# Kernel tuning notes

Hardware: AMD Instinct MI355X
Metric: run time of the kernel (lower is better)

Reference implementation:

```python
import jax, jax.numpy as jnp
import numpy as np

L_LAYERS = 6   # decoder layers
N_HEAD = 8
NUM_PAIR = 100  # num_pair_queries
LN_EPS = 1e-5


def _ln(x, g, b):
    m = x.mean(-1, keepdims=True)
    v = ((x - m) ** 2).mean(-1, keepdims=True)
    return (x - m) / jnp.sqrt(v + LN_EPS) * g + b


def _mlp2(x, w1, b1, w2, b2):
    return jax.nn.relu(x @ w1.T + b1) @ w2.T + b2


def _mha(q, k, v, in_w, in_b, out_w, out_b):
    # torch nn.MultiheadAttention (batch_first, eval mode) equivalent
    C = q.shape[-1]
    dh = C // N_HEAD
    wq, wk, wv = jnp.split(in_w, 3, axis=0)
    bq, bk, bv = jnp.split(in_b, 3, axis=0)
    def heads(x, w, b):
        y = x @ w.T + b
        return y.reshape(x.shape[0], x.shape[1], N_HEAD, dh).transpose(0, 2, 1, 3)
    qh, kh, vh = heads(q, wq, bq), heads(k, wk, bk), heads(v, wv, bv)
    att = jax.nn.softmax(jnp.einsum('bhqd,bhkd->bhqk', qh, kh) * (1.0 / np.sqrt(dh)), axis=-1)
    out = jnp.einsum('bhqk,bhkd->bhqd', att, vh).transpose(0, 2, 1, 3).reshape(q.shape[0], q.shape[1], C)
    return out @ out_w.T + out_b


def reference(hs_last, mem, mem_pos, sub_boxes, obj_boxes,
              su_w1, su_b1, su_w2, su_b2, ou_w1, ou_b1, ou_w2, ou_b2,
              pm_w1, pm_b1, pm_w2, pm_b2, sp_w1, sp_b1, sp_w2, sp_b2,
              sa_in_w, sa_in_b, sa_out_w, sa_out_b, ca_in_w, ca_in_b, ca_out_w, ca_out_b,
              l1_w, l1_b, l2_w, l2_b, n1_g, n1_b, n2_g, n2_b, n3_g, n3_b):
    B, Q, C = hs_last.shape
    N = Q // 2
    hsp = hs_last.reshape(B, N, 2, C)
    sub_feat, obj_feat = hsp[:, :, 0, :], hsp[:, :, 1, :]

    # --- HumanObjectPairLearner.select_topk_indices (mapper='identity') ---
    sub_emb = _mlp2(sub_feat, su_w1, su_b1, su_w2, su_b2)
    obj_emb = _mlp2(obj_feat, ou_w1, ou_b1, ou_w2, ou_b2)
    sub_emb = sub_emb / (jnp.linalg.norm(sub_emb, axis=-1, keepdims=True) + 1e-6)
    obj_emb = obj_emb / (jnp.linalg.norm(obj_emb, axis=-1, keepdims=True) + 1e-6)
    importance = jnp.einsum('bnc,bmc->bnm', sub_emb, obj_emb)  # [B, N, N]
    K = min(NUM_PAIR, N * N)
    _, idx = jax.lax.top_k(importance.reshape(B, N * N), K)
    sub_pos, obj_pos = idx // N, idx % N  # [B, K]

    # --- build_pair_queries: gather selected sub/obj features ---
    sel_sub = jnp.take_along_axis(sub_feat, sub_pos[:, :, None], axis=1)  # [B, K, C]
    sel_obj = jnp.take_along_axis(obj_feat, obj_pos[:, :, None], axis=1)
    pair_q = _mlp2(jnp.concatenate([sel_sub, sel_obj], axis=-1), pm_w1, pm_b1, pm_w2, pm_b2)

    # --- PairSpatialEncoding ---
    sp = _mlp2(jnp.concatenate([sub_boxes, obj_boxes], axis=-1), sp_w1, sp_b1, sp_w2, sp_b2)

    # --- LocalityAwareInteractionDecoder (eval mode: dropout = identity) ---
    q = pair_q
    k_mem = mem + mem_pos
    for i in range(L_LAYERS):
        q_sp = q + sp
        sa = _mha(q_sp, q_sp, q_sp, sa_in_w[i], sa_in_b[i], sa_out_w[i], sa_out_b[i])
        q = _ln(q + sa, n1_g[i], n1_b[i])
        # original: cross_attn(cat([q, sp], dim=1), ...)[:, :K] -- attention is
        # per-query, so slicing after equals running cross-attn with q alone.
        ca = _mha(q, k_mem, mem, ca_in_w[i], ca_in_b[i], ca_out_w[i], ca_out_b[i])
        q = _ln(q + ca, n2_g[i], n2_b[i])
        ffn = jax.nn.relu(q @ l1_w[i].T + l1_b[i]) @ l2_w[i].T + l2_b[i]
        q = _ln(q + ffn, n3_g[i], n3_b[i])
    return q


def setup_inputs() -> dict:
    B, N, C, M, F, L = 32, 100, 256, 4096, 2048, L_LAYERS
    K = NUM_PAIR
    keys = iter(jax.random.split(jax.random.key(0), 80))
    def nrm(shape, s=1.0):
        return jax.random.normal(next(keys), shape, jnp.float32) * s
    w = lambda shape: nrm(shape, 0.02)
    return {
        'hs_last': nrm((B, 2 * N, C)),
        'mem': nrm((B, M, C)),
        'mem_pos': nrm((B, M, C)),
        'sub_boxes': jax.random.uniform(next(keys), (B, K, 4), jnp.float32),
        'obj_boxes': jax.random.uniform(next(keys), (B, K, 4), jnp.float32),
        'su_w1': w((C, C)), 'su_b1': jnp.zeros((C,)), 'su_w2': w((C, C)), 'su_b2': jnp.zeros((C,)),
        'ou_w1': w((C, C)), 'ou_b1': jnp.zeros((C,)), 'ou_w2': w((C, C)), 'ou_b2': jnp.zeros((C,)),
        'pm_w1': w((C, 2 * C)), 'pm_b1': jnp.zeros((C,)), 'pm_w2': w((C, C)), 'pm_b2': jnp.zeros((C,)),
        'sp_w1': w((C, 8)), 'sp_b1': jnp.zeros((C,)), 'sp_w2': w((C, C)), 'sp_b2': jnp.zeros((C,)),
        'sa_in_w': w((L, 3 * C, C)), 'sa_in_b': jnp.zeros((L, 3 * C)),
        'sa_out_w': w((L, C, C)), 'sa_out_b': jnp.zeros((L, C)),
        'ca_in_w': w((L, 3 * C, C)), 'ca_in_b': jnp.zeros((L, 3 * C)),
        'ca_out_w': w((L, C, C)), 'ca_out_b': jnp.zeros((L, C)),
        'l1_w': w((L, F, C)), 'l1_b': jnp.zeros((L, F)),
        'l2_w': w((L, C, F)), 'l2_b': jnp.zeros((L, C)),
        'n1_g': jnp.ones((L, C)), 'n1_b': jnp.zeros((L, C)),
        'n2_g': jnp.ones((L, C)), 'n2_b': jnp.zeros((L, C)),
        'n3_g': jnp.ones((L, C)), 'n3_b': jnp.zeros((L, C)),
    }
```

## Files before the change

kernel.cpp:

```cpp
#include <hip/hip_runtime.h>
#include <hip/hip_bf16.h>

#define Bb 32
#define Nn 100
#define Cc 256
#define Mm 4096
#define Ff 2048
#define Ll 6
#define Hh 8
#define DH 32
#define KP 100
#define TT (Bb*KP)
#define LNEPS 1e-5f
#define NCH 4
#define SUBK 128

typedef __hip_bfloat16 bf16;
typedef unsigned short ushort_t;
typedef __attribute__((ext_vector_type(8))) short short8v;
typedef __attribute__((ext_vector_type(4))) float f32x4;

union FragU { uint2 u2[2]; uint4 u4; short8v s8; };

__device__ __forceinline__ float bfu2f(unsigned short u) {
  union { unsigned u32; float f; } cv; cv.u32 = ((unsigned)u) << 16; return cv.f;
}
__device__ __forceinline__ unsigned short f2bf(float f) {
  union { float f; unsigned u; } c; c.f = f;
  unsigned r = c.u + 0x7FFF + ((c.u >> 16) & 1);
  return (unsigned short)(r >> 16);
}
__device__ __forceinline__ unsigned pack2(float a, float b) {
  return (unsigned)f2bf(a) | ((unsigned)f2bf(b) << 16);
}

__global__ __launch_bounds__(256) void gemm_kv(
    const bf16* __restrict__ Ak, const bf16* __restrict__ Wk,
    const float* __restrict__ bk, bf16* __restrict__ outK,
    const bf16* __restrict__ Avv, const bf16* __restrict__ Wv,
    const float* __restrict__ bv, bf16* __restrict__ outV,
    const float* __restrict__ Aq, const bf16* __restrict__ Wq,
    const float* __restrict__ bq, bf16* __restrict__ outQ)
{
  __shared__ ushort_t Ct[128*136];
  const int nwgK = ((Bb*Mm) >> 7) * 2;
  const int nwgQ = (TT >> 7) * 2;
  const int nwg = 2*nwgK + nwgQ;
  const int g = blockIdx.x;
  const int xcd = g & 7, lid = g >> 3;
  const int q8 = nwg >> 3, r8 = nwg & 7;
  int wgid = (xcd < r8 ? xcd*(q8+1) : r8*(q8+1) + (xcd - r8)*q8) + lid;
  int seg;
  const bf16* A = nullptr; const bf16* W; const float* bias; bf16* out;
  if (wgid < nwgK)        { seg = 0; A = Ak;  W = Wk; bias = bk; out = outK; }
  else if (wgid < 2*nwgK) { seg = 1; wgid -= nwgK;   A = Avv; W = Wv; bias = bv; out = outV; }
  else                    { seg = 2; wgid -= 2*nwgK; W = Wq; bias = bq; out = outQ; }
  const int ntile = wgid & 1, mtile = wgid >> 1;
  const int bm = mtile << 7, bn = ntile << 7;
  const int tid = threadIdx.x;
  const int w = tid >> 6, lane = tid & 63;
  const int lr = lane & 15, lg = lane >> 4;
  const int wm = w >> 1, wn = w & 1;

  f32x4 acc[4][4] = {};

  if (seg != 2) {
    #pragma unroll 2
    for (int k0 = 0; k0 < Cc; k0 += 32) {
      FragU a[4], b[4];
      #pragma unroll
      for (int mi = 0; mi < 4; ++mi)
        a[mi].u4 = *(const uint4*)(A + (size_t)(bm + wm*64 + mi*16 + lr)*Cc + k0 + lg*8);
      #pragma unroll
      for (int ni = 0; ni < 4; ++ni)
        b[ni].u4 = *(const uint4*)(W + (size_t)(bn + wn*64 + ni*16 + lr)*Cc + k0 + lg*8);
      #pragma unroll
      for (int ni = 0; ni < 4; ++ni)
        #pragma unroll
        for (int mi = 0; mi < 4; ++mi)
          acc[mi][ni] = __builtin_amdgcn_mfma_f32_16x16x32_bf16(a[mi].s8, b[ni].s8,
                                                                acc[mi][ni], 0, 0, 0);
    }
  } else {
    #pragma unroll 2
    for (int k0 = 0; k0 < Cc; k0 += 32) {
      FragU a[4], b[4];
      #pragma unroll
      for (int mi = 0; mi < 4; ++mi) {
        const float* ap = Aq + (size_t)(bm + wm*64 + mi*16 + lr)*Cc + k0 + lg*8;
        float4 f0 = *(const float4*)ap;
        float4 f1 = *(const float4*)(ap + 4);
        a[mi].u4.x = pack2(f0.x, f0.y); a[mi].u4.y = pack2(f0.z, f0.w);
        a[mi].u4.z = pack2(f1.x, f1.y); a[mi].u4.w = pack2(f1.z, f1.w);
      }
      #pragma unroll
      for (int ni = 0; ni < 4; ++ni)
        b[ni].u4 = *(const uint4*)(W + (size_t)(bn + wn*64 + ni*16 + lr)*Cc + k0 + lg*8);
      #pragma unroll
      for (int ni = 0; ni < 4; ++ni)
        #pragma unroll
        for (int mi = 0; mi < 4; ++mi)
          acc[mi][ni] = __builtin_amdgcn_mfma_f32_16x16x32_bf16(a[mi].s8, b[ni].s8,
                                                                acc[mi][ni], 0, 0, 0);
    }
  }

  const float scale = (seg == 2) ? 0.17677669529663687f : 1.f;
  #pragma unroll
  for (int ni = 0; ni < 4; ++ni) {
    int col = wn*64 + ni*16 + lr;
    float bvv = bias[bn + col];
    #pragma unroll
    for (int mi = 0; mi < 4; ++mi)
      #pragma unroll
      for (int r = 0; r < 4; ++r) {
        int rowl = wm*64 + mi*16 + lg*4 + r;
        Ct[rowl*136 + col] = f2bf((acc[mi][ni][r] + bvv) * scale);
      }
  }
  __syncthreads();
  for (int u = tid; u < 2048; u += 256) {
    int rowl = u >> 4, sub = u & 15;
    uint4 v = *(const uint4*)&Ct[rowl*136 + sub*8];
    int m = bm + rowl;
    int gcol = bn + sub*8;
    int h = gcol >> 5, dd = gcol & 31;
    if (seg != 2) {
      int bb = m >> 12, mm = m & 4095;
      *(uint4*)(out + (((size_t)bb*Hh + h)*Mm + mm)*DH + dd) = v;
    } else {
      int bb = m / KP, qq = m % KP;
      *(uint4*)(out + (((size_t)bb*Hh + h)*KP + qq)*DH + dd) = v;
    }
  }
}

template<int AT, bool RELU, int OM>
__global__ __launch_bounds__(256) void gemm_mfma(
    const void* __restrict__ Av, const float* __restrict__ A2,
    const bf16* __restrict__ W, const float* __restrict__ bias,
    void* __restrict__ out, int M, int N, int K)
{
  __shared__ ushort_t SM[2*128*72];
  ushort_t* As = SM;
  ushort_t* Bs = SM + 128*72;
  const int mt = M >> 7, nt = N >> 7;
  const int nwg = mt * nt;
  const int g = blockIdx.x;
  const int xcd = g & 7, lid = g >> 3;
  const int q8 = nwg >> 3, r8 = nwg & 7;
  int wgid = (xcd < r8 ? xcd*(q8+1) : r8*(q8+1) + (xcd - r8)*q8) + lid;
  const int ntile = wgid % nt, mtile = wgid / nt;
  const int bm = mtile << 7, bn = ntile << 7;
  const int tid = threadIdx.x;
  const int w = tid >> 6, lane = tid & 63;
  const int lr = lane & 15, lg = lane >> 4;
  const int wm = w >> 1, wn = w & 1;
  const float* Af = (const float*)Av;
  const bf16*  Ab = (const bf16*)Av;

  f32x4 acc[4][4] = {};

  for (int k0 = 0; k0 < K; k0 += 64) {
    __syncthreads();
    #pragma unroll
    for (int i = 0; i < 4; ++i) {
      int linear = i*256 + tid;
      int row = linear >> 3, c8 = linear & 7;
      uint4 packed;
      if (AT == 0) {
        const float* ap = Af + (size_t)(bm+row)*K + k0 + c8*8;
        float4 f0 = *(const float4*)ap;
        float4 f1 = *(const float4*)(ap+4);
        if (A2) {
          const float* ap2 = A2 + (size_t)(bm+row)*K + k0 + c8*8;
          float4 g0 = *(const float4*)ap2;
          float4 g1 = *(const float4*)(ap2+4);
          f0.x += g0.x; f0.y += g0.y; f0.z += g0.z; f0.w += g0.w;
          f1.x += g1.x; f1.y += g1.y; f1.z += g1.z; f1.w += g1.w;
        }
        packed.x = pack2(f0.x, f0.y); packed.y = pack2(f0.z, f0.w);
        packed.z = pack2(f1.x, f1.y); packed.w = pack2(f1.z, f1.w);
      } else {
        packed = *(const uint4*)(Ab + (size_t)(bm+row)*K + k0 + c8*8);
      }
      *(uint4*)&As[row*72 + c8*8] = packed;
      uint4 wb = *(const uint4*)(W + (size_t)(bn+row)*K + k0 + c8*8);
      *(uint4*)&Bs[row*72 + c8*8] = wb;
    }
    __syncthreads();
    #pragma unroll
    for (int kk = 0; kk < 64; kk += 32) {
      FragU a[4];
      #pragma unroll
      for (int mi = 0; mi < 4; ++mi)
        a[mi].u4 = *(const uint4*)&As[(wm*64 + mi*16 + lr)*72 + kk + lg*8];
      #pragma unroll
      for (int ni = 0; ni < 4; ++ni) {
        FragU bfr;
        bfr.u4 = *(const uint4*)&Bs[(wn*64 + ni*16 + lr)*72 + kk + lg*8];
        #pragma unroll
        for (int mi = 0; mi < 4; ++mi)
          acc[mi][ni] = __builtin_amdgcn_mfma_f32_16x16x32_bf16(a[mi].s8, bfr.s8,
                                                                acc[mi][ni], 0, 0, 0);
      }
    }
  }

  #pragma unroll
  for (int ni = 0; ni < 4; ++ni) {
    int col = bn + wn*64 + ni*16 + lr;
    float bv = bias ? bias[col] : 0.f;
    #pragma unroll
    for (int mi = 0; mi < 4; ++mi) {
      #pragma unroll
      for (int r = 0; r < 4; ++r) {
        int m = bm + wm*64 + mi*16 + lg*4 + r;
        float v = acc[mi][ni][r] + bv;
        if (RELU) v = fmaxf(v, 0.f);
        if (OM == 0) {
          ((float*)out)[(size_t)m*N + col] = v;
        } else if (OM == 1) {
          ((bf16*)out)[(size_t)m*N + col] = __float2bfloat16(v);
        } else {
          int bb = m / KP, qq = m % KP;
          int h = col >> 5, dd = col & 31;
          ((bf16*)out)[(((size_t)bb*Hh + h)*KP + qq)*DH + dd] =
              __float2bfloat16(v * 0.17677669529663687f);
        }
      }
    }
  }
}

template<int AT>
__global__ __launch_bounds__(512) void gemm_ln(
    const void* __restrict__ Av, const bf16* __restrict__ W,
    const float* __restrict__ bias, const float* __restrict__ resid,
    const float* __restrict__ gamma, const float* __restrict__ beta,
    float* __restrict__ out, int M, int K,
    const bf16* __restrict__ part, const float2* __restrict__ ml)
{
  __shared__ ushort_t As[16][72];
  __shared__ ushort_t Bs[256][72];
  __shared__ float redS[16][8];
  __shared__ float redQ[16][8];
  const int bm = blockIdx.x * 16;
  const int tid = threadIdx.x;
  const int w = tid >> 6, lane = tid & 63;
  const int lr = lane & 15, lg = lane >> 4;
  const float* Af = (const float*)Av;
  const bf16*  Ab = (const bf16*)Av;
  f32x4 acc[2] = {};

  for (int k0 = 0; k0 < K; k0 += 64) {
    __syncthreads();
    if (tid < 128) {
      int row = tid >> 3, c8 = tid & 7;
      uint4 packed;
      if (AT == 0) {
        const float* ap = Af + (size_t)(bm+row)*K + k0 + c8*8;
        float4 f0 = *(const float4*)ap;
        float4 f1 = *(const float4*)(ap+4);
        packed.x = pack2(f0.x, f0.y); packed.y = pack2(f0.z, f0.w);
        packed.z = pack2(f1.x, f1.y); packed.w = pack2(f1.z, f1.w);
      } else if (AT == 1) {
        packed = *(const uint4*)(Ab + (size_t)(bm+row)*K + k0 + c8*8);
      } else {
        int t = bm + row;
        int b = t / KP, q = t % KP;
        int ch0 = k0 + c8*8;
        int h = ch0 >> 5, d0 = ch0 & 31;
        int bh = b*Hh + h;
        float2 m0 = ml[((size_t)bh*NCH + 0)*KP + q];
        float2 m1 = ml[((size_t)bh*NCH + 1)*KP + q];
        float2 m2 = ml[((size_t)bh*NCH + 2)*KP + q];
        float2 m3 = ml[((size_t)bh*NCH + 3)*KP + q];
        float mm = fmaxf(fmaxf(m0.x, m1.x), fmaxf(m2.x, m3.x));
        float w0 = __expf(m0.x - mm), w1 = __expf(m1.x - mm);
        float w2 = __expf(m2.x - mm), w3 = __expf(m3.x - mm);
        float invL = 1.f / (m0.y*w0 + m1.y*w1 + m2.y*w2 + m3.y*w3);
        float o[8] = {};
        float wc[NCH] = { w0, w1, w2, w3 };
        #pragma unroll
        for (int c = 0; c < NCH; ++c) {
          uint4 pv = *(const uint4*)(part + (((size_t)bh*NCH + c)*KP + q)*DH + d0);
          const ushort_t* pe = (const ushort_t*)&pv;
          #pragma unroll
          for (int e = 0; e < 8; ++e) o[e] += wc[c] * bfu2f(pe[e]);
        }
        packed.x = pack2(o[0]*invL, o[1]*invL);
        packed.y = pack2(o[2]*invL, o[3]*invL);
        packed.z = pack2(o[4]*invL, o[5]*invL);
        packed.w = pack2(o[6]*invL, o[7]*invL);
      }
      *(uint4*)&As[row][c8*8] = packed;
    }
    #pragma unroll
    for (int i = 0; i < 4; ++i) {
      int linear = i*512 + tid;
      int row = linear >> 3, c8 = linear & 7;
      *(uint4*)&Bs[row][c8*8] = *(const uint4*)(W + (size_t)row*K + k0 + c8*8);
    }
    __syncthreads();
    #pragma unroll
    for (int kk = 0; kk < 64; kk += 32) {
      FragU a;
      a.u4 = *(const uint4*)&As[lr][kk + lg*8];
      #pragma unroll
      for (int ni = 0; ni < 2; ++ni) {
        FragU bfr;
        bfr.u4 = *(const uint4*)&Bs[w*32 + ni*16 + lr][kk + lg*8];
        acc[ni] = __builtin_amdgcn_mfma_f32_16x16x32_bf16(a.s8, bfr.s8, acc[ni], 0, 0, 0);
      }
    }
  }

  float x[2][4];
  #pragma unroll
  for (int r = 0; r < 4; ++r) {
    int row = bm + lg*4 + r;
    float s = 0.f, sq = 0.f;
    #pragma unroll
    for (int ni = 0; ni < 2; ++ni) {
      int col = w*32 + ni*16 + lr;
      float v = acc[ni][r] + bias[col] + resid[(size_t)row*Cc + col];
      x[ni][r] = v;
      s += v; sq += v*v;
    }
    #pragma unroll
    for (int m2 = 1; m2 < 16; m2 <<= 1) { s += __shfl_xor(s, m2); sq += __shfl_xor(sq, m2); }
    if (lr == 0) { redS[lg*4 + r][w] = s; redQ[lg*4 + r][w] = sq; }
  }
  __syncthreads();
  #pragma unroll
  for (int r = 0; r < 4; ++r) {
    int lrow = lg*4 + r;
    float ss = 0.f, sq = 0.f;
    #pragma unroll
    for (int j = 0; j < 8; ++j) { ss += redS[lrow][j]; sq += redQ[lrow][j]; }
    float mean = ss * (1.f/Cc);
    float var = sq * (1.f/Cc) - mean*mean;
    float inv = rsqrtf(var + LNEPS);
    #pragma unroll
    for (int ni = 0; ni < 2; ++ni) {
      int col = w*32 + ni*16 + lr;
      out[(size_t)(bm+lrow)*Cc + col] = (x[ni][r] - mean)*inv*gamma[col] + beta[col];
    }
  }
}

#define NSEG 9
struct CvtDesc {
  const float* src[NSEG];
  bf16* dst[NSEG];
  int n4[NSEG];
  int total4;
};
__global__ __launch_bounds__(256) void cvt_multi(CvtDesc d) {
  int stride = gridDim.x * blockDim.x;
  for (int i = blockIdx.x*256 + threadIdx.x; i < d.total4; i += stride) {
    int seg = 0, off = i;
    while (off >= d.n4[seg]) { off -= d.n4[seg]; ++seg; }
    float4 f = *(const float4*)(d.src[seg] + (size_t)off*4);
    uint2 p; p.x = pack2(f.x, f.y); p.y = pack2(f.z, f.w);
    *(uint2*)(d.dst[seg] + (size_t)off*4) = p;
  }
}

__global__ __launch_bounds__(256) void prep_mem(const float4* __restrict__ mem4,
                                                const float4* __restrict__ pos4,
                                                uint2* __restrict__ kb2,
                                                uint2* __restrict__ vb2) {
  int i = blockIdx.x*256 + threadIdx.x;
  const int stride = 8192*256;
  #pragma unroll
  for (int t = 0; t < 4; ++t) {
    int j = i + t*stride;
    float4 a = mem4[j];
    float4 p = pos4[j];
    uint2 vv; vv.x = pack2(a.x, a.y); vv.y = pack2(a.z, a.w);
    uint2 kv; kv.x = pack2(a.x + p.x, a.y + p.y); kv.y = pack2(a.z + p.z, a.w + p.w);
    vb2[j] = vv;
    kb2[j] = kv;
  }
}

template<bool RELU>
__global__ __launch_bounds__(256) void gemm_nt(
    const float* __restrict__ A0, const float* __restrict__ W0,
    const float* __restrict__ b0, float* __restrict__ o0,
    const float* __restrict__ A1, const float* __restrict__ W1,
    const float* __restrict__ b1, float* __restrict__ o1,
    int M, int N, int K)
{
  const float* A = blockIdx.z ? A1 : A0;
  const float* Wt = blockIdx.z ? W1 : W0;
  const float* bias = blockIdx.z ? b1 : b0;
  float* out = blockIdx.z ? o1 : o0;
  __shared__ float As[16][68];
  __shared__ float Ws[16][68];
  const int bm = blockIdx.y * 64, bn = blockIdx.x * 64;
  const int tid = threadIdx.x;
  const int kk = tid & 15, rr = tid >> 4;
  const int tx = tid & 15, ty = tid >> 4;
  float acc[4][4] = {};
  for (int k0 = 0; k0 < K; k0 += 16) {
    #pragma unroll
    for (int p = 0; p < 4; ++p) {
      int m = rr + p*16;
      int row = bm + m;
      float av = 0.f, wv = 0.f;
      bool kin = (k0 + kk) < K;
      if (row < M && kin) av = A[(size_t)row * K + k0 + kk];
      int wrow = bn + m;
      if (wrow < N && kin) wv = Wt[(size_t)wrow * K + k0 + kk];
      As[kk][m] = av;
      Ws[kk][m] = wv;
    }
    __syncthreads();
    #pragma unroll
    for (int q = 0; q < 16; ++q) {
      float a[4], w[4];
      #pragma unroll
      for (int i = 0; i < 4; ++i) a[i] = As[q][ty*4 + i];
      #pragma unroll
      for (int j = 0; j < 4; ++j) w[j] = Ws[q][tx*4 + j];
      #pragma unroll
      for (int i = 0; i < 4; ++i)
        #pragma unroll
        for (int j = 0; j < 4; ++j) acc[i][j] += a[i] * w[j];
    }
    __syncthreads();
  }
  #pragma unroll
  for (int i = 0; i < 4; ++i) {
    int row = bm + ty*4 + i;
    if (row >= M) continue;
    #pragma unroll
    for (int j = 0; j < 4; ++j) {
      int col = bn + tx*4 + j;
      if (col >= N) continue;
      float v = acc[i][j];
      if (bias) v += bias[col];
      if (RELU) v = v > 0.f ? v : 0.f;
      out[(size_t)row*N + col] = v;
    }
  }
}

__global__ void split_subobj(const float* __restrict__ hs,
                             float* __restrict__ subf, float* __restrict__ objf) {
  int i = blockIdx.x*256 + threadIdx.x;
  if (i >= Bb*Nn*Cc) return;
  int c = i % Cc, n = (i / Cc) % Nn, b = i / (Cc*Nn);
  subf[i] = hs[((size_t)b*2*Nn + 2*n    )*Cc + c];
  objf[i] = hs[((size_t)b*2*Nn + 2*n + 1)*Cc + c];
}

__global__ __launch_bounds__(256) void l2norm_kernel(float* __restrict__ x) {
  int t = blockIdx.x, c = threadIdx.x;
  float v = x[(size_t)t*Cc + c];
  __shared__ float red[256];
  red[c] = v*v; __syncthreads();
  for (int s = 128; s > 0; s >>= 1) { if (c < s) red[c] += red[c+s]; __syncthreads(); }
  float scale = 1.f / (sqrtf(red[0]) + 1e-6f);
  x[(size_t)t*Cc + c] = v * scale;
}

__global__ __launch_bounds__(128) void importance_kernel(const float* __restrict__ se,
                                                         const float* __restrict__ oe,
                                                         float* __restrict__ imp) {
  int b = blockIdx.x / Nn, n = blockIdx.x % Nn;
  int m = threadIdx.x;
  if (m >= Nn) return;
  const float* s = se + ((size_t)b*Nn + n)*Cc;
  const float* o = oe + ((size_t)b*Nn + m)*Cc;
  float acc = 0.f;
  for (int c = 0; c < Cc; ++c) acc += s[c] * o[c];
  imp[((size_t)b*Nn + n)*Nn + m] = acc;
}

__global__ __launch_bounds__(1024) void topk_kernel(const float* __restrict__ imp,
                                                    int* __restrict__ idx_out) {
  __shared__ unsigned mu[Nn*Nn];
  __shared__ unsigned hist[256];
  __shared__ unsigned prefix;
  __shared__ int remK;
  __shared__ unsigned long long keys[128];
  __shared__ unsigned tiebuf[256];
  __shared__ unsigned cnt_gt, cnt_tie;
  const int b = blockIdx.x, tid = threadIdx.x;
  const int NN = Nn*Nn;

  for (int i = tid; i < NN; i += 1024) {
    unsigned u = __float_as_uint(imp[(size_t)b*NN + i]);
    mu[i] = (u & 0x80000000u) ? ~u : (u | 0x80000000u);
  }
  if (tid == 0) { prefix = 0u; remK = KP; cnt_gt = 0u; cnt_tie = 0u; }
  __syncthreads();

  for (int shift = 24; shift >= 0; shift -= 8) {
    if (tid < 256) hist[tid] = 0u;
    __syncthreads();
    unsigned pmask = (shift == 24) ? 0u : (0xFFFFFFFFu << (shift + 8));
    unsigned pref = prefix;
    for (int i = tid; i < NN; i += 1024) {
      unsigned v = mu[i];
      if ((v & pmask) == pref) atomicAdd(&hist[(v >> shift) & 0xFFu], 1u);
    }
    __syncthreads();
    if (tid == 0) {
      int rk = remK;
      unsigned sel = 0u;
      for (int bin = 255; bin >= 0; --bin) {
        int c = (int)hist[bin];
        if (c >= rk) { sel = (unsigned)bin; break; }
        rk -= c;
      }
      remK = rk;
      prefix = pref | (sel << shift);
    }
    __syncthreads();
  }

  const unsigned T = prefix;
  const int need = remK;

  for (int i = tid; i < NN; i += 1024) {
    unsigned v = mu[i];
    if (v > T) {
      unsigned p = atomicAdd(&cnt_gt, 1u);
      keys[p] = ((unsigned long long)(~v) << 32) | (unsigned)i;
    } else if (v == T) {
      unsigned p = atomicAdd(&cnt_tie, 1u);
      if (p < 256u) tiebuf[p] = (unsigned)i;
    }
  }
  __syncthreads();
  const unsigned ngt = cnt_gt;
  const unsigned nt_ = cnt_tie < 256u ? cnt_tie : 256u;

  for (int i = tid; i < 256; i += 1024) if (i >= (int)nt_) tiebuf[i] = 0xFFFFFFFFu;
  __syncthreads();
  for (int ksz = 2; ksz <= 256; ksz <<= 1) {
    for (int st = ksz >> 1; st > 0; st >>= 1) {
      if (tid < 128) {
        int i = ((tid & ~(st-1)) << 1) | (tid & (st-1));
        int j = i | st;
        bool up = ((i & ksz) == 0);
        unsigned a = tiebuf[i], c = tiebuf[j];
        if ((a > c) == up) { tiebuf[i] = c; tiebuf[j] = a; }
      }
      __syncthreads();
    }
  }
  for (int t = tid; t < need; t += 1024)
    keys[ngt + t] = ((unsigned long long)(~T) << 32) | tiebuf[t];
  for (int i = tid; i < 128; i += 1024)
    if (i >= KP) keys[i] = 0xFFFFFFFFFFFFFFFFull;
  __syncthreads();

  for (int ksz = 2; ksz <= 128; ksz <<= 1) {
    for (int st = ksz >> 1; st > 0; st >>= 1) {
      if (tid < 64) {
        int i = ((tid & ~(st-1)) << 1) | (tid & (st-1));
        int j = i | st;
        bool up = ((i & ksz) == 0);
        unsigned long long a = keys[i], c = keys[j];
        if ((a > c) == up) { keys[i] = c; keys[j] = a; }
      }
      __syncthreads();
    }
  }
  if (tid < KP) idx_out[b*KP + tid] = (int)(keys[tid] & 0xFFFFFFFFu);
}

__global__ __launch_bounds__(256) void gather_pair(const float* __restrict__ subf,
                                                   const float* __restrict__ objf,
                                                   const int* __restrict__ idx,
                                                   float* __restrict__ pc) {
  int bk = blockIdx.x;
  int b = bk / KP;
  int id = idx[bk];
  int spos = id / Nn, opos = id % Nn;
  const float* s = subf + ((size_t)b*Nn + spos)*Cc;
  const float* o = objf + ((size_t)b*Nn + opos)*Cc;
  float* dst = pc + (size_t)bk * (2*Cc);
  for (int c = threadIdx.x; c < Cc; c += 256) { dst[c] = s[c]; dst[Cc + c] = o[c]; }
}

__global__ void boxes_cat_kernel(const float* __restrict__ sb, const float* __restrict__ ob,
                                 float* __restrict__ out) {
  int i = blockIdx.x*256 + threadIdx.x;
  if (i >= TT*8) return;
  int c = i & 7, bk = i >> 3;
  out[i] = (c < 4) ? sb[bk*4 + c] : ob[bk*4 + (c - 4)];
}

__global__ __launch_bounds__(512) void attn_sa(const bf16* __restrict__ qkv,
                                               float* __restrict__ out) {
  __shared__ float Kt[128][36];
  __shared__ float Vt[128][36];
  __shared__ float Qs[KP][DH];
  __shared__ float Ps[8][128];
  int bh = blockIdx.x; int b = bh >> 3, h = bh & 7;
  int tid = threadIdx.x;
  const float scale = 0.17677669529663687f;
  const size_t base = (size_t)b * KP * (3*Cc);
  for (int i = tid; i < KP*DH; i += 512) {
    int q = i >> 5, d = i & 31;
    Qs[q][d] = __bfloat162float(qkv[base + (size_t)q*(3*Cc) + h*DH + d]) * scale;
  }
  {
    int j = tid >> 2, qc = tid & 3;
    float kf[8], vf[8];
    if (j < KP) {
      uint4 kraw = *(const uint4*)(qkv + base + (size_t)j*(3*Cc) + Cc   + h*DH + qc*8);
      uint4 vraw = *(const uint4*)(qkv + base + (size_t)j*(3*Cc) + 2*Cc + h*DH + qc*8);
      const ushort_t* ks = (const ushort_t*)&kraw;
      const ushort_t* vs = (const ushort_t*)&vraw;
      #pragma unroll
      for (int e = 0; e < 8; ++e) { kf[e] = bfu2f(ks[e]); vf[e] = bfu2f(vs[e]); }
    } else {
      #pragma unroll
      for (int e = 0; e < 8; ++e) { kf[e] = 0.f; vf[e] = 0.f; }
    }
    ((float4*)Kt[j])[qc*2]   = make_float4(kf[0],kf[1],kf[2],kf[3]);
    ((float4*)Kt[j])[qc*2+1] = make_float4(kf[4],kf[5],kf[6],kf[7]);
    ((float4*)Vt[j])[qc*2]   = make_float4(vf[0],vf[1],vf[2],vf[3]);
    ((float4*)Vt[j])[qc*2+1] = make_float4(vf[4],vf[5],vf[6],vf[7]);
  }
  __syncthreads();
  int w = tid >> 6, lane = tid & 63;
  int d = lane & 31, half = lane >> 5;
  for (int q = w; q < KP; q += 8) {
    float s0 = 0.f, s1 = 0.f;
    #pragma unroll
    for (int c = 0; c < 8; ++c) {
      float4 k0 = ((const float4*)Kt[lane])[c];
      float4 k1 = ((const float4*)Kt[lane+64])[c];
      float4 qv = *(const float4*)&Qs[q][c*4];
      s0 += k0.x*qv.x + k0.y*qv.y + k0.z*qv.z + k0.w*qv.w;
      s1 += k1.x*qv.x + k1.y*qv.y + k1.z*qv.z + k1.w*qv.w;
    }
    if (lane >= KP) s0 = -1e30f;
    if (lane + 64 >= KP) s1 = -1e30f;
    float mx = fmaxf(s0, s1);
    #pragma unroll
    for (int m2 = 32; m2 > 0; m2 >>= 1) mx = fmaxf(mx, __shfl_xor(mx, m2));
    float p0 = (lane < KP)      ? expf(s0 - mx) : 0.f;
    float p1 = (lane + 64 < KP) ? expf(s1 - mx) : 0.f;
    float sm = p0 + p1;
    #pragma unroll
    for (int m2 = 32; m2 > 0; m2 >>= 1) sm += __shfl_xor(sm, m2);
    Ps[w][lane] = p0; Ps[w][lane+64] = p1;
    float pv = 0.f;
    for (int s = 0; s < 64; ++s) {
      int j = half*64 + s;
      pv += Ps[w][j] * Vt[j][d];
    }
    pv += __shfl_xor(pv, 32);
    if (lane < 32) out[((size_t)b*KP + q)*Cc + h*DH + d] = pv / sm;
  }
}

__global__ __launch_bounds__(256) void attn_ca_mfma(
    const bf16* __restrict__ qhH,
    const bf16* __restrict__ khH,
    const bf16* __restrict__ vhH,
    bf16* __restrict__ part,
    float2* __restrict__ ml)
{
  __shared__ unsigned short Vs[32][140];
  const int bx = blockIdx.x;
  const int bh = bx >> 2, ch = bx & 3;
  const int tid = threadIdx.x;
  const int w = tid >> 6, lane = tid & 63;
  const int lr = lane & 15, lg = lane >> 4;
  const int k0base = ch * (Mm / NCH);
  const int qt0 = w, qt1 = w + 4;

  FragU qf[2];
  {
    int r0 = qt0*16 + lr;
    qf[0].u4 = *(const uint4*)(qhH + ((size_t)bh*KP + r0)*DH + lg*8);
    int r1 = qt1*16 + lr;
    if (r1 < KP) qf[1].u4 = *(const uint4*)(qhH + ((size_t)bh*KP + r1)*DH + lg*8);
    else         qf[1].u4 = make_uint4(0u,0u,0u,0u);
  }

  f32x4 acc[2][2] = {};
  float mreg[2] = {-1e30f, -1e30f};
  float lreg[2] = {0.f, 0.f};

  const int srcA = (2*(lg & 1))*16 + lr;
  const int srcB = srcA + 16;
  const bool hi_kt = (lg >> 1) != 0;

  for (int sc = 0; sc < (Mm/NCH)/SUBK; ++sc) {
    const int k0 = k0base + sc*SUBK;
    __syncthreads();
    {
      int p2 = tid & 63, c = tid >> 6;
      uint4 v0 = *(const uint4*)(vhH + ((size_t)bh*Mm + k0 + 2*p2    )*DH + c*8);
      uint4 v1 = *(const uint4*)(vhH + ((size_t)bh*Mm + k0 + 2*p2 + 1)*DH + c*8);
      const unsigned short* a0 = (const unsigned short*)&v0;
      const unsigned short* a1 = (const unsigned short*)&v1;
      #pragma unroll
      for (int e = 0; e < 8; ++e) {
        int d = c*8 + e;
        *(unsigned int*)&Vs[d][2*p2] = (unsigned)a0[e] | ((unsigned)a1[e] << 16);
      }
    }
    FragU kf[8];
    #pragma unroll
    for (int kt = 0; kt < 8; ++kt)
      kf[kt].u4 = *(const uint4*)(khH + ((size_t)bh*Mm + k0 + kt*16 + lr)*DH + lg*8);
    __syncthreads();

    #pragma unroll
    for (int j = 0; j < 2; ++j) {
      f32x4 sv[8];
      __builtin_amdgcn_s_setprio(1);
      #pragma unroll
      for (int kt = 0; kt < 8; ++kt) {
        f32x4 z = {0.f, 0.f, 0.f, 0.f};
        sv[kt] = __builtin_amdgcn_mfma_f32_16x16x32_bf16(kf[kt].s8, qf[j].s8, z, 0, 0, 0);
      }
      __builtin_amdgcn_s_setprio(0);
      float mx = -1e30f;
      #pragma unroll
      for (int kt = 0; kt < 8; ++kt)
        mx = fmaxf(mx, fmaxf(fmaxf(sv[kt][0], sv[kt][1]), fmaxf(sv[kt][2], sv[kt][3])));
      mx = fmaxf(mx, __shfl_xor(mx, 16));
      mx = fmaxf(mx, __shfl_xor(mx, 32));
      float newm = fmaxf(mreg[j], mx);
      float resc = __expf(mreg[j] - newm);
      mreg[j] = newm;
      float psum = 0.f;
      unsigned pl[8], ph[8];
      #pragma unroll
      for (int kt = 0; kt < 8; ++kt) {
        float p0 = __expf(sv[kt][0] - newm);
        float p1 = __expf(sv[kt][1] - newm);
        float p2 = __expf(sv[kt][2] - newm);
        float p3 = __expf(sv[kt][3] - newm);
        psum += (p0 + p1) + (p2 + p3);
        pl[kt] = pack2(p0, p1);
        ph[kt] = pack2(p2, p3);
      }
      psum += __shfl_xor(psum, 16);
      psum += __shfl_xor(psum, 32);
      lreg[j] = lreg[j]*resc + psum;
      #pragma unroll
      for (int dt = 0; dt < 2; ++dt)
        #pragma unroll
        for (int r = 0; r < 4; ++r) acc[j][dt][r] *= resc;

      #pragma unroll
      for (int ks = 0; ks < 4; ++ks) {
        unsigned aA = __shfl(pl[2*ks],   srcA), bA = __shfl(pl[2*ks+1], srcA);
        unsigned aB = __shfl(ph[2*ks],   srcA), bB = __shfl(ph[2*ks+1], srcA);
        unsigned cA = __shfl(pl[2*ks],   srcB), dA = __shfl(pl[2*ks+1], srcB);
        unsigned cB = __shfl(ph[2*ks],   srcB), dB = __shfl(ph[2*ks+1], srcB);
        FragU pf;
        pf.u4.x = hi_kt ? bA : aA;
        pf.u4.y = hi_kt ? bB : aB;
        pf.u4.z = hi_kt ? dA : cA;
        pf.u4.w = hi_kt ? dB : cB;
        __builtin_amdgcn_s_setprio(1);
        #pragma unroll
        for (int dt = 0; dt < 2; ++dt) {
          FragU vf;
          vf.u2[0] = *(const uint2*)&Vs[dt*16 + lr][ks*32 + lg*8];
          vf.u2[1] = *(const uint2*)&Vs[dt*16 + lr][ks*32 + lg*8 + 4];
          acc[j][dt] = __builtin_amdgcn_mfma_f32_16x16x32_bf16(vf.s8, pf.s8,
                                                               acc[j][dt], 0, 0, 0);
        }
        __builtin_amdgcn_s_setprio(0);
      }
    }
  }

  #pragma unroll
  for (int j = 0; j < 2; ++j) {
    int q = (j ? qt1 : qt0)*16 + lr;
    if (q < KP) {
      if (lg == 0) ml[((size_t)bh*NCH + ch)*KP + q] = make_float2(mreg[j], lreg[j]);
      #pragma unroll
      for (int dt = 0; dt < 2; ++dt)
        #pragma unroll
        for (int r = 0; r < 4; ++r) {
          int d = dt*16 + lg*4 + r;
          part[(((size_t)bh*NCH + ch)*KP + q)*DH + d] = __float2bfloat16(acc[j][dt][r]);
        }
    }
  }
}

extern "C" void kernel_launch(void* const* d_in, const int* in_sizes, int n_in,
                              void* d_out, int out_size, void* d_ws, size_t ws_size,
                              hipStream_t stream) {
  auto in = [&](int i) { return (const float*)d_in[i]; };
  const float* hs        = in(0);
  const float* mem       = in(1);
  const float* mem_pos   = in(2);
  const float* sub_boxes = in(3);
  const float* obj_boxes = in(4);
  const float* su_w1 = in(5),  *su_b1 = in(6),  *su_w2 = in(7),  *su_b2 = in(8);
  const float* ou_w1 = in(9),  *ou_b1 = in(10), *ou_w2 = in(11), *ou_b2 = in(12);
  const float* pm_w1 = in(13), *pm_b1 = in(14), *pm_w2 = in(15), *pm_b2 = in(16);
  const float* sp_w1 = in(17), *sp_b1 = in(18), *sp_w2 = in(19), *sp_b2 = in(20);
  const float* sa_in_w = in(21),  *sa_in_b = in(22), *sa_out_w = in(23), *sa_out_b = in(24);
  const float* ca_in_w = in(25),  *ca_in_b = in(26), *ca_out_w = in(27), *ca_out_b = in(28);
  const float* l1_w = in(29), *l1_b = in(30), *l2_w = in(31), *l2_b = in(32);
  const float* n1_g = in(33), *n1_b = in(34), *n2_g = in(35), *n2_b = in(36);
  const float* n3_g = in(37), *n3_b = in(38);

  char* wsp = (char*)d_ws;
  auto alloc = [&](size_t bytes) { char* p = wsp; wsp += (bytes + 255) & ~(size_t)255; return p; };
  bf16* khH = (bf16*)alloc((size_t)Bb*Mm*Cc*2);
  bf16* vhH = (bf16*)alloc((size_t)Bb*Mm*Cc*2);
  bf16* kmem_b = (bf16*)alloc((size_t)Bb*Mm*Cc*2);
  bf16* vmem_b = (bf16*)alloc((size_t)Bb*Mm*Cc*2);
  bf16* qhH = (bf16*)alloc((size_t)TT*Cc*2);
  bf16* part = (bf16*)alloc((size_t)Bb*Hh*NCH*KP*DH*2);
  float2* mlbuf = (float2*)alloc((size_t)Bb*Hh*NCH*KP*8);
  bf16* sawb = (bf16*)alloc((size_t)Ll*3*Cc*Cc*2);
  bf16* cawb = (bf16*)alloc((size_t)Ll*3*Cc*Cc*2);
  bf16* sowb = (bf16*)alloc((size_t)Ll*Cc*Cc*2);
  bf16* cowb = (bf16*)alloc((size_t)Ll*Cc*Cc*2);
  bf16* l1wb = (bf16*)alloc((size_t)Ll*Ff*Cc*2);
  bf16* l2wb = (bf16*)alloc((size_t)Ll*Cc*Ff*2);
  bf16* pm1b = (bf16*)alloc((size_t)Cc*2*Cc*2);
  bf16* pm2b = (bf16*)alloc((size_t)Cc*Cc*2);
  bf16* spw2b = (bf16*)alloc((size_t)Cc*Cc*2);
  float* subf    = (float*)alloc((size_t)Bb*Nn*Cc*4);
  float* objf    = (float*)alloc((size_t)Bb*Nn*Cc*4);
  float* sub_emb = (float*)alloc((size_t)Bb*Nn*Cc*4);
  float* obj_emb = (float*)alloc((size_t)Bb*Nn*Cc*4);
  float* embh    = (float*)alloc((size_t)TT*2*Cc*4);
  float* embh2   = (float*)alloc((size_t)TT*Cc*4);
  float* imp     = (float*)alloc((size_t)Bb*Nn*Nn*4);
  int*   idx     = (int*)  alloc((size_t)Bb*KP*4);
  float* pair_cat= (float*)alloc((size_t)TT*2*Cc*4);
  float* bxc     = (float*)alloc((size_t)TT*8*4);
  float* spb     = (float*)alloc((size_t)TT*Cc*4);
  float* qbuf    = (float*)alloc((size_t)TT*Cc*4);
  bf16*  qkvb    = (bf16*)alloc((size_t)TT*3*Cc*2);
  float* attn_o  = (float*)alloc((size_t)TT*Cc*4);
  bf16*  ffnb    = (bf16*)alloc((size_t)TT*Ff*2);

  {
    CvtDesc d;
    const float* srcs[NSEG] = { sa_in_w, ca_in_w, sa_out_w, ca_out_w, l1_w, l2_w, pm_w1, pm_w2, sp_w2 };
    bf16* dsts[NSEG] = { sawb, cawb, sowb, cowb, l1wb, l2wb, pm1b, pm2b, spw2b };
    size_t ns[NSEG] = { (size_t)Ll*3*Cc*Cc, (size_t)Ll*3*Cc*Cc, (size_t)Ll*Cc*Cc,
                        (size_t)Ll*Cc*Cc, (size_t)Ll*Ff*Cc, (size_t)Ll*Cc*Ff,
                        (size_t)Cc*2*Cc, (size_t)Cc*Cc, (size_t)Cc*Cc };
    int tot = 0;
    for (int i = 0; i < NSEG; ++i) { d.src[i] = srcs[i]; d.dst[i] = dsts[i]; d.n4[i] = (int)(ns[i]/4); tot += d.n4[i]; }
    d.total4 = tot;
    cvt_multi<<<2048, 256, 0, stream>>>(d);
  }
  prep_mem<<<8192, 256, 0, stream>>>((const float4*)mem, (const float4*)mem_pos,
                                     (uint2*)kmem_b, (uint2*)vmem_b);

  auto GFP = [&](const float* A0, const float* W0, const float* b0, float* o0,
                 const float* A1, const float* W1, const float* b1, float* o1,
                 int M, int N, int K, bool relu, int zz) {
    dim3 g((N + 63)/64, (M + 63)/64, zz), t(256);
    if (relu) gemm_nt<true ><<<g, t, 0, stream>>>(A0,W0,b0,o0,A1,W1,b1,o1,M,N,K);
    else      gemm_nt<false><<<g, t, 0, stream>>>(A0,W0,b0,o0,A1,W1,b1,o1,M,N,K);
  };

  auto GM = [&](const void* A, const float* A2, const bf16* W, const float* bias,
                void* out, int M, int N, int K, int OM, bool relu) {
    int blocks = (M >> 7) * (N >> 7);
    if (OM == 0) {
      if (relu) gemm_mfma<0,true ,0><<<blocks,256,0,stream>>>(A,A2,W,bias,out,M,N,K);
      else      gemm_mfma<0,false,0><<<blocks,256,0,stream>>>(A,A2,W,bias,out,M,N,K);
    } else if (OM == 1) {
      if (relu) gemm_mfma<0,true ,1><<<blocks,256,0,stream>>>(A,A2,W,bias,out,M,N,K);
      else      gemm_mfma<0,false,1><<<blocks,256,0,stream>>>(A,A2,W,bias,out,M,N,K);
    } else {
      gemm_mfma<0,false,3><<<blocks,256,0,stream>>>(A,A2,W,bias,out,M,N,K);
    }
  };

  split_subobj<<<(Bb*Nn*Cc + 255)/256, 256, 0, stream>>>(hs, subf, objf);
  GFP(subf, su_w1, su_b1, embh,  objf,  ou_w1, ou_b1, embh2, TT, Cc, Cc, true,  2);
  GFP(embh, su_w2, su_b2, sub_emb, embh2, ou_w2, ou_b2, obj_emb, TT, Cc, Cc, false, 2);
  l2norm_kernel<<<2*TT, 256, 0, stream>>>(sub_emb);
  importance_kernel<<<Bb*Nn, 128, 0, stream>>>(sub_emb, obj_emb, imp);
  topk_kernel<<<Bb, 1024, 0, stream>>>(imp, idx);
  gather_pair<<<TT, 256, 0, stream>>>(subf, objf, idx, pair_cat);
  GM(pair_cat, nullptr, pm1b, pm_b1, embh, TT, Cc, 2*Cc, 0, true);
  GM(embh,     nullptr, pm2b, pm_b2, qbuf, TT, Cc, Cc,   0, false);
  boxes_cat_kernel<<<(TT*8 + 255)/256, 256, 0, stream>>>(sub_boxes, obj_boxes, bxc);
  GFP(bxc,  sp_w1, sp_b1, embh, nullptr,nullptr,nullptr,nullptr, TT, Cc, 8,  true,  1);
  GM(embh, nullptr, spw2b, sp_b2, spb, TT, Cc, Cc, 0, false);

  for (int i = 0; i < Ll; ++i) {
    const bf16* sawL = sawb + (size_t)i*3*Cc*Cc;
    const bf16* cawL = cawb + (size_t)i*3*Cc*Cc;
    const float* sab = sa_in_b + (size_t)i*3*Cc;
    const float* cab = ca_in_b + (size_t)i*3*Cc;

    GM(qbuf, spb, sawL, sab, qkvb, TT, 3*Cc, Cc, 1, false);
    attn_sa<<<Bb*Hh, 512, 0, stream>>>(qkvb, attn_o);
    gemm_ln<0><<<TT/16, 512, 0, stream>>>(attn_o, sowb + (size_t)i*Cc*Cc,
        sa_out_b + (size_t)i*Cc, qbuf, n1_g + i*Cc, n1_b + i*Cc, qbuf, TT, Cc,
        nullptr, nullptr);

    gemm_kv<<<1074, 256, 0, stream>>>(
        kmem_b, cawL + (size_t)Cc*Cc,   cab + Cc,   khH,
        vmem_b, cawL + (size_t)2*Cc*Cc, cab + 2*Cc, vhH,
        qbuf,   cawL,                   cab,        qhH);
    attn_ca_mfma<<<Bb*Hh*NCH, 256, 0, stream>>>(qhH, khH, vhH, part, mlbuf);
    gemm_ln<2><<<TT/16, 512, 0, stream>>>(nullptr, cowb + (size_t)i*Cc*Cc,
        ca_out_b + (size_t)i*Cc, qbuf, n2_g + i*Cc, n2_b + i*Cc, qbuf, TT, Cc,
        part, mlbuf);

    GM(qbuf, nullptr, l1wb + (size_t)i*Ff*Cc, l1_b + (size_t)i*Ff, ffnb, TT, Ff, Cc, 1, true);
    float* qo = (i == Ll-1) ? (float*)d_out : qbuf;
    gemm_ln<1><<<TT/16, 512, 0, stream>>>(ffnb, l2wb + (size_t)i*Cc*Ff,
        l2_b + (size_t)i*Cc, qbuf, n3_g + i*Cc, n3_b + i*Cc, qo, TT, Ff,
        nullptr, nullptr);
  }
}
```

Before: 1.693 ms.

## Fuse FFN up-projection, ReLU, down-projection and LayerNorm into one kernel

Result: slower. 1.741 ms (+2.8%).

```diff
diff --git a/kernel.cpp b/kernel.cpp
--- a/kernel.cpp
+++ b/kernel.cpp
@@ -19,6 +19,8 @@
 typedef unsigned short ushort_t;
 typedef __attribute__((ext_vector_type(8))) short short8v;
 typedef __attribute__((ext_vector_type(4))) float f32x4;
+typedef __attribute__((ext_vector_type(4))) float f4v;
+typedef __attribute__((ext_vector_type(2))) unsigned u2v;
 
 union FragU { uint2 u2[2]; uint4 u4; short8v s8; };
 
@@ -250,7 +252,6 @@
   const int w = tid >> 6, lane = tid & 63;
   const int lr = lane & 15, lg = lane >> 4;
   const float* Af = (const float*)Av;
-  const bf16*  Ab = (const bf16*)Av;
   f32x4 acc[2] = {};
 
   for (int k0 = 0; k0 < K; k0 += 64) {
@@ -264,8 +265,6 @@
         float4 f1 = *(const float4*)(ap+4);
         packed.x = pack2(f0.x, f0.y); packed.y = pack2(f0.z, f0.w);
         packed.z = pack2(f1.x, f1.y); packed.w = pack2(f1.z, f1.w);
-      } else if (AT == 1) {
-        packed = *(const uint4*)(Ab + (size_t)(bm+row)*K + k0 + c8*8);
       } else {
         int t = bm + row;
         int b = t / KP, q = t % KP;
@@ -350,6 +349,106 @@
   }
 }
 
+__global__ __launch_bounds__(512) void ffn_ln(
+    const float* __restrict__ A, const bf16* __restrict__ W1,
+    const float* __restrict__ b1, const bf16* __restrict__ W2,
+    const float* __restrict__ b2, const float* __restrict__ resid,
+    const float* __restrict__ gamma, const float* __restrict__ beta,
+    float* __restrict__ out, int M)
+{
+  __shared__ ushort_t As[16*264];
+  __shared__ ushort_t Hs[16*264];
+  __shared__ float redS[16][8];
+  __shared__ float redQ[16][8];
+  const int bm = blockIdx.x * 16;
+  const int tid = threadIdx.x;
+  const int w = tid >> 6, lane = tid & 63;
+  const int lr = lane & 15, lg = lane >> 4;
+
+  {
+    int row = tid >> 5, c8 = tid & 31;
+    const float* ap = A + (size_t)(bm+row)*Cc + c8*8;
+    float4 f0 = *(const float4*)ap;
+    float4 f1 = *(const float4*)(ap+4);
+    uint4 packed;
+    packed.x = pack2(f0.x, f0.y); packed.y = pack2(f0.z, f0.w);
+    packed.z = pack2(f1.x, f1.y); packed.w = pack2(f1.z, f1.w);
+    *(uint4*)&As[row*264 + c8*8] = packed;
+  }
+  __syncthreads();
+
+  f32x4 acc2[2] = {};
+
+  for (int hc = 0; hc < Ff; hc += 256) {
+    f32x4 h[2] = {};
+    #pragma unroll
+    for (int kk = 0; kk < Cc; kk += 32) {
+      FragU a;
+      a.u4 = *(const uint4*)&As[lr*264 + kk + lg*8];
+      #pragma unroll
+      for (int ni = 0; ni < 2; ++ni) {
+        FragU bfr;
+        bfr.u4 = *(const uint4*)(W1 + (size_t)(hc + w*32 + ni*16 + lr)*Cc + kk + lg*8);
+        h[ni] = __builtin_amdgcn_mfma_f32_16x16x32_bf16(a.s8, bfr.s8, h[ni], 0, 0, 0);
+      }
+    }
+    __syncthreads();
+    #pragma unroll
+    for (int ni = 0; ni < 2; ++ni) {
+      int col = w*32 + ni*16 + lr;
+      float bvv = b1[hc + col];
+      #pragma unroll
+      for (int r = 0; r < 4; ++r)
+        Hs[(lg*4 + r)*264 + col] = f2bf(fmaxf(h[ni][r] + bvv, 0.f));
+    }
+    __syncthreads();
+    #pragma unroll
+    for (int kk = 0; kk < 256; kk += 32) {
+      FragU ha;
+      ha.u4 = *(const uint4*)&Hs[lr*264 + kk + lg*8];
+      #pragma unroll
+      for (int ni = 0; ni < 2; ++ni) {
+        FragU bfr;
+        bfr.u4 = *(const uint4*)(W2 + (size_t)(w*32 + ni*16 + lr)*Ff + hc + kk + lg*8);
+        acc2[ni] = __builtin_amdgcn_mfma_f32_16x16x32_bf16(ha.s8, bfr.s8, acc2[ni], 0, 0, 0);
+      }
+    }
+  }
+
+  float x[2][4];
+  #pragma unroll
+  for (int r = 0; r < 4; ++r) {
+    int row = bm + lg*4 + r;
+    float s = 0.f, sq = 0.f;
+    #pragma unroll
+    for (int ni = 0; ni < 2; ++ni) {
+      int col = w*32 + ni*16 + lr;
+      float v = acc2[ni][r] + b2[col] + resid[(size_t)row*Cc + col];
+      x[ni][r] = v;
+      s += v; sq += v*v;
+    }
+    #pragma unroll
+    for (int m2 = 1; m2 < 16; m2 <<= 1) { s += __shfl_xor(s, m2); sq += __shfl_xor(sq, m2); }
+    if (lr == 0) { redS[lg*4 + r][w] = s; redQ[lg*4 + r][w] = sq; }
+  }
+  __syncthreads();
+  #pragma unroll
+  for (int r = 0; r < 4; ++r) {
+    int lrow = lg*4 + r;
+    float ss = 0.f, sq = 0.f;
+    #pragma unroll
+    for (int j = 0; j < 8; ++j) { ss += redS[lrow][j]; sq += redQ[lrow][j]; }
+    float mean = ss * (1.f/Cc);
+    float var = sq * (1.f/Cc) - mean*mean;
+    float inv = rsqrtf(var + LNEPS);
+    #pragma unroll
+    for (int ni = 0; ni < 2; ++ni) {
+      int col = w*32 + ni*16 + lr;
+      out[(size_t)(bm+lrow)*Cc + col] = (x[ni][r] - mean)*inv*gamma[col] + beta[col];
+    }
+  }
+}
+
 #define NSEG 9
 struct CvtDesc {
   const float* src[NSEG];
@@ -368,21 +467,22 @@
   }
 }
 
-__global__ __launch_bounds__(256) void prep_mem(const float4* __restrict__ mem4,
-                                                const float4* __restrict__ pos4,
-                                                uint2* __restrict__ kb2,
-                                                uint2* __restrict__ vb2) {
+__global__ __launch_bounds__(256) void prep_mem(const f4v* __restrict__ mem4,
+                                                const f4v* __restrict__ pos4,
+                                                u2v* __restrict__ kb2,
+                                                u2v* __restrict__ vb2) {
   int i = blockIdx.x*256 + threadIdx.x;
   const int stride = 8192*256;
   #pragma unroll
   for (int t = 0; t < 4; ++t) {
     int j = i + t*stride;
-    float4 a = mem4[j];
-    float4 p = pos4[j];
-    uint2 vv; vv.x = pack2(a.x, a.y); vv.y = pack2(a.z, a.w);
-    uint2 kv; kv.x = pack2(a.x + p.x, a.y + p.y); kv.y = pack2(a.z + p.z, a.w + p.w);
-    vb2[j] = vv;
-    kb2[j] = kv;
+    f4v a = __builtin_nontemporal_load(&mem4[j]);
+    f4v p = __builtin_nontemporal_load(&pos4[j]);
+    u2v vv, kv;
+    vv.x = pack2(a.x, a.y); vv.y = pack2(a.z, a.w);
+    kv.x = pack2(a.x + p.x, a.y + p.y); kv.y = pack2(a.z + p.z, a.w + p.w);
+    __builtin_nontemporal_store(vv, &vb2[j]);
+    __builtin_nontemporal_store(kv, &kb2[j]);
   }
 }
 
@@ -850,7 +950,6 @@
   float* qbuf    = (float*)alloc((size_t)TT*Cc*4);
   bf16*  qkvb    = (bf16*)alloc((size_t)TT*3*Cc*2);
   float* attn_o  = (float*)alloc((size_t)TT*Cc*4);
-  bf16*  ffnb    = (bf16*)alloc((size_t)TT*Ff*2);
 
   {
     CvtDesc d;
@@ -864,8 +963,8 @@
     d.total4 = tot;
     cvt_multi<<<2048, 256, 0, stream>>>(d);
   }
-  prep_mem<<<8192, 256, 0, stream>>>((const float4*)mem, (const float4*)mem_pos,
-                                     (uint2*)kmem_b, (uint2*)vmem_b);
+  prep_mem<<<8192, 256, 0, stream>>>((const f4v*)mem, (const f4v*)mem_pos,
+                                     (u2v*)kmem_b, (u2v*)vmem_b);
 
   auto GFP = [&](const float* A0, const float* W0, const float* b0, float* o0,
                  const float* A1, const float* W1, const float* b1, float* o1,
@@ -923,10 +1022,9 @@
         ca_out_b + (size_t)i*Cc, qbuf, n2_g + i*Cc, n2_b + i*Cc, qbuf, TT, Cc,
         part, mlbuf);
 
-    GM(qbuf, nullptr, l1wb + (size_t)i*Ff*Cc, l1_b + (size_t)i*Ff, ffnb, TT, Ff, Cc, 1, true);
     float* qo = (i == Ll-1) ? (float*)d_out : qbuf;
-    gemm_ln<1><<<TT/16, 512, 0, stream>>>(ffnb, l2wb + (size_t)i*Cc*Ff,
-        l2_b + (size_t)i*Cc, qbuf, n3_g + i*Cc, n3_b + i*Cc, qo, TT, Ff,
-        nullptr, nullptr);
-  }
-}
+    ffn_ln<<<TT/16, 512, 0, stream>>>(qbuf, l1wb + (size_t)i*Ff*Cc,
+        l1_b + (size_t)i*Ff, l2wb + (size_t)i*Cc*Ff, l2_b + (size_t)i*Cc,
+        qbuf, n3_g + i*Cc, n3_b + i*Cc, qo, TT);
+  }
+}
```
